# Kernel optimization log

Hardware: AMD Instinct MI355X
Metric: run time of the kernel (lower is better)

Reference implementation:

```python
import jax, jax.numpy as jnp
import numpy as np

N_EXPERTS, D_IN, D_OUT = 8, 1024, 1024
N_TOKENS = 8192


def setup_inputs() -> dict:
    key = jax.random.key(0)
    ks = jax.random.split(key, 5)
    s_in = 1.0 / np.sqrt(D_IN)
    x = jax.random.normal(ks[0], (N_TOKENS, D_IN), dtype=jnp.float32)
    W = jax.random.uniform(ks[1], (N_EXPERTS, D_IN, D_OUT), jnp.float32, -s_in, s_in)
    b = jax.random.uniform(ks[2], (N_EXPERTS, D_OUT), jnp.float32, -s_in, s_in)
    gate_W = jax.random.uniform(ks[3], (D_IN, N_EXPERTS), jnp.float32, -s_in, s_in)
    gate_b = jax.random.uniform(ks[4], (N_EXPERTS,), jnp.float32, -s_in, s_in)
    return {"x": x, "W": W, "b": b, "gate_W": gate_W, "gate_b": gate_b}


def reference(x, W, b, gate_W, gate_b):
    # gate: [n, e] softmax over experts
    gate_score = jax.nn.softmax(x @ gate_W + gate_b, axis=-1)
    # all experts applied densely: [n, e, o]
    expert_outputs = jnp.einsum('ni,eio->neo', x, W) + b[None, :, :]
    # weighted combine over expert axis: [n, o]
    return jnp.einsum('ne,neo->no', gate_score, expert_outputs)
```

## Files before the change

### kernel.cpp

```cpp
#include <hip/hip_runtime.h>
#include <hip/hip_bf16.h>
#include <cstdint>
#include <cstddef>

#define N_TOK 8192
#define D_IN  1024
#define D_OUT 1024
#define N_EXP 8
#define KTOT  (N_EXP * D_IN)

typedef __attribute__((ext_vector_type(8))) short short8;
typedef __attribute__((ext_vector_type(8))) unsigned short ushort8;
typedef __attribute__((ext_vector_type(4))) float f32x4;

__device__ __forceinline__ unsigned short f2bf(float f) {
    union { float f; unsigned int u; } v; v.f = f;
    return (unsigned short)((v.u + 0x7FFFu + ((v.u >> 16) & 1u)) >> 16);
}

__device__ __forceinline__ void load_lds16(const void* g, void* l) {
    __builtin_amdgcn_global_load_lds(
        (const __attribute__((address_space(1))) void*)g,
        (__attribute__((address_space(3))) void*)l,
        16, 0, 0);
}

__global__ __launch_bounds__(256) void prep_kernel(
    const float* __restrict__ x, const float* __restrict__ gW,
    const float* __restrict__ gbias, const float* __restrict__ W,
    unsigned short* __restrict__ xb, unsigned short* __restrict__ Wt,
    float* __restrict__ g_t) {
    const int b = blockIdx.x;
    const int t = threadIdx.x;

    if (b < 2048) {
        __shared__ float tile[64][65];
        const int e  = b >> 8;
        const int i0 = ((b >> 4) & 15) * 64;
        const int o0 = (b & 15) * 64;

        const int rr = t >> 4;
        const int rc = (t & 15) * 4;
#pragma unroll
        for (int j = 0; j < 4; ++j) {
            const float4 v = *(const float4*)(
                W + ((size_t)e * D_IN + (i0 + rr + 16 * j)) * D_OUT + o0 + rc);
            tile[rr + 16 * j][rc + 0] = v.x;
            tile[rr + 16 * j][rc + 1] = v.y;
            tile[rr + 16 * j][rc + 2] = v.z;
            tile[rr + 16 * j][rc + 3] = v.w;
        }
        __syncthreads();
        const int ow = t >> 2;
        const int c  = (t & 3) * 16;
        ushort8 v0, v1;
#pragma unroll
        for (int j = 0; j < 8; ++j) v0[j] = f2bf(tile[c + j][ow]);
#pragma unroll
        for (int j = 0; j < 8; ++j) v1[j] = f2bf(tile[c + 8 + j][ow]);
        unsigned short* dst = Wt + (size_t)(o0 + ow) * KTOT + e * D_IN + i0 + c;
        *(ushort8*)dst = v0;
        *(ushort8*)(dst + 8) = v1;
    } else {
        const int lane = t & 63;
        const int n    = (b - 2048) * 4 + (t >> 6);

        float acc[8];
#pragma unroll
        for (int e = 0; e < 8; ++e) acc[e] = 0.f;
#pragma unroll
        for (int jj = 0; jj < 4; ++jj) {
            const int i = 256 * jj + 4 * lane;
            const float4 xv = *(const float4*)(x + (size_t)n * D_IN + i);
            ushort4 u;
            u.x = f2bf(xv.x); u.y = f2bf(xv.y);
            u.z = f2bf(xv.z); u.w = f2bf(xv.w);
            *(ushort4*)(xb + (size_t)n * D_IN + i) = u;
            const float xs[4] = {xv.x, xv.y, xv.z, xv.w};
#pragma unroll
            for (int j = 0; j < 4; ++j) {
                const float* wr = gW + (size_t)(i + j) * N_EXP;
                const float4 w0 = *(const float4*)wr;
                const float4 w1 = *(const float4*)(wr + 4);
                acc[0] += xs[j] * w0.x; acc[1] += xs[j] * w0.y;
                acc[2] += xs[j] * w0.z; acc[3] += xs[j] * w0.w;
                acc[4] += xs[j] * w1.x; acc[5] += xs[j] * w1.y;
                acc[6] += xs[j] * w1.z; acc[7] += xs[j] * w1.w;
            }
        }
#pragma unroll
        for (int off = 32; off > 0; off >>= 1) {
#pragma unroll
            for (int e = 0; e < 8; ++e) acc[e] += __shfl_down(acc[e], off);
        }
        if (lane == 0) {
            float lg[8], mx = -1e30f;
#pragma unroll
            for (int e = 0; e < 8; ++e) {
                lg[e] = acc[e] + gbias[e];
                mx = fmaxf(mx, lg[e]);
            }
            float s = 0.f;
#pragma unroll
            for (int e = 0; e < 8; ++e) { lg[e] = expf(lg[e] - mx); s += lg[e]; }
            const float inv = 1.f / s;
#pragma unroll
            for (int e = 0; e < 8; ++e)
                g_t[(size_t)e * N_TOK + n] = lg[e] * inv;
        }
    }
}

__global__ __launch_bounds__(256, 2) void moe_gemm6_kernel(
    const unsigned short* __restrict__ xb,
    const unsigned short* __restrict__ Wt,
    const float* __restrict__ bias,
    const float* __restrict__ g_t,
    float* __restrict__ out) {
    __shared__ __align__(16) unsigned short Abuf[2][128 * 32];
    __shared__ __align__(16) unsigned short Bbuf[2][128 * 32];
    __shared__ __align__(16) float g_s[N_EXP][128];
    __shared__ __align__(16) float r_s[N_EXP][128];
    __shared__ __align__(16) float b_s[N_EXP][128];

    const int t    = threadIdx.x;
    const int lane = t & 63;
    const int ln15 = lane & 15;
    const int quad = lane >> 4;
    const int wave = t >> 6;
    const int wm0  = (wave >> 1) * 64;
    const int wn0  = (wave & 1) * 64;

    const int flat = blockIdx.x + 8 * blockIdx.y;
    const int xs_  = (flat >> 3) & 7;
    const int ys_  = ((flat & 7) << 3) | (flat >> 6);
    const int bn0  = xs_ * 128;
    const int bm0  = ys_ * 128;

    for (int j = t; j < N_EXP * 128; j += 256) {
        const int e = j >> 7, r = j & 127;
        g_s[e][r] = g_t[(size_t)e * N_TOK + bm0 + r];
        b_s[e][r] = bias[(size_t)e * D_OUT + bn0 + r];
    }
    __syncthreads();
    if (t < 128) {
        float d[N_EXP];
#pragma unroll
        for (int e = 0; e < N_EXP; ++e) d[e] = fmaxf(g_s[e][t], 1e-30f);
#pragma unroll
        for (int e = 1; e < N_EXP; ++e) r_s[e][t] = d[e - 1] / d[e];
        r_s[0][t] = d[N_EXP - 1];
    }

    f32x4 acc[4][4];
#pragma unroll
    for (int mi = 0; mi < 4; ++mi)
#pragma unroll
        for (int ni = 0; ni < 4; ++ni)
            acc[mi][ni] = (f32x4){0.f, 0.f, 0.f, 0.f};

    unsigned short* aL0[2] = {&Abuf[0][wave * 512], &Abuf[1][wave * 512]};
    unsigned short* aL1[2] = {&Abuf[0][2048 + wave * 512],
                              &Abuf[1][2048 + wave * 512]};
    unsigned short* bL0[2] = {&Bbuf[0][wave * 512], &Bbuf[1][wave * 512]};
    unsigned short* bL1[2] = {&Bbuf[0][2048 + wave * 512],
                              &Bbuf[1][2048 + wave * 512]};

    const int csw = ((t & 3) ^ ((t >> 3) & 3)) * 8;
    const unsigned short* ga =
        xb + (size_t)(bm0 + (t >> 2)) * D_IN + csw;
    const unsigned short* gbB =
        Wt + (size_t)(bn0 + (t >> 2)) * KTOT + csw;

    const int ksw = (quad ^ ((ln15 >> 1) & 3)) * 8;

    load_lds16(ga, aL0[0]);
    load_lds16(ga + 64 * D_IN, aL1[0]);
    load_lds16(gbB, bL0[0]);
    load_lds16(gbB + 64 * KTOT, bL1[0]);
    __syncthreads();

    for (int kt = 0; kt < 256; ++kt) {
        const int cb  = kt & 1;
        const int nb  = cb ^ 1;
        const int kt1 = (kt + 1) & 255;

        load_lds16(ga + (kt1 & 31) * 32,              aL0[nb]);
        load_lds16(ga + 64 * D_IN + (kt1 & 31) * 32,  aL1[nb]);
        load_lds16(gbB + kt1 * 32,                    bL0[nb]);
        load_lds16(gbB + 64 * KTOT + kt1 * 32,        bL1[nb]);

        if (kt && !(kt & 31)) {
            const int e = kt >> 5;
#pragma unroll
            for (int mi = 0; mi < 4; ++mi) {
                const f32x4 rv = *(const f32x4*)&r_s[e][wm0 + mi * 16 + quad * 4];
#pragma unroll
                for (int ni = 0; ni < 4; ++ni)
#pragma unroll
                    for (int r = 0; r < 4; ++r) acc[mi][ni][r] *= rv[r];
            }
        }

        short8 af[4], bv[4];
#pragma unroll
        for (int mi = 0; mi < 4; ++mi)
            af[mi] = *(const short8*)
                &Abuf[cb][(wm0 + mi * 16 + ln15) * 32 + ksw];
#pragma unroll
        for (int ni = 0; ni < 4; ++ni)
            bv[ni] = *(const short8*)
                &Bbuf[cb][(wn0 + ni * 16 + ln15) * 32 + ksw];
#pragma unroll
        for (int mi = 0; mi < 4; ++mi)
#pragma unroll
            for (int ni = 0; ni < 4; ++ni)
                acc[mi][ni] = __builtin_amdgcn_mfma_f32_16x16x32_bf16(
                    af[mi], bv[ni], acc[mi][ni], 0, 0, 0);

        __syncthreads();
    }

#pragma unroll
    for (int mi = 0; mi < 4; ++mi) {
        const f32x4 fin = *(const f32x4*)&r_s[0][wm0 + mi * 16 + quad * 4];
#pragma unroll
        for (int ni = 0; ni < 4; ++ni)
#pragma unroll
            for (int r = 0; r < 4; ++r) acc[mi][ni][r] *= fin[r];
    }
#pragma unroll
    for (int e = 0; e < N_EXP; ++e) {
        f32x4 gv[4];
        float bv[4];
#pragma unroll
        for (int mi = 0; mi < 4; ++mi)
            gv[mi] = *(const f32x4*)&g_s[e][wm0 + mi * 16 + quad * 4];
#pragma unroll
        for (int ni = 0; ni < 4; ++ni) bv[ni] = b_s[e][wn0 + ni * 16 + ln15];
#pragma unroll
        for (int mi = 0; mi < 4; ++mi)
#pragma unroll
            for (int ni = 0; ni < 4; ++ni)
#pragma unroll
                for (int r = 0; r < 4; ++r)
                    acc[mi][ni][r] += gv[mi][r] * bv[ni];
    }

#pragma unroll
    for (int mi = 0; mi < 4; ++mi) {
#pragma unroll
        for (int ni = 0; ni < 4; ++ni) {
            const int col  = bn0 + wn0 + ni * 16 + ln15;
            const int row0 = bm0 + wm0 + mi * 16 + quad * 4;
#pragma unroll
            for (int r = 0; r < 4; ++r)
                out[(size_t)(row0 + r) * D_OUT + col] = acc[mi][ni][r];
        }
    }
}

extern "C" void kernel_launch(void* const* d_in, const int* in_sizes, int n_in,
                              void* d_out, int out_size, void* d_ws, size_t ws_size,
                              hipStream_t stream) {
    const float* x  = (const float*)d_in[0];
    const float* W  = (const float*)d_in[1];
    const float* b  = (const float*)d_in[2];
    const float* gW = (const float*)d_in[3];
    const float* gb = (const float*)d_in[4];
    float* out = (float*)d_out;

    unsigned short* xb  = (unsigned short*)d_ws;
    unsigned short* Wt  = xb + (size_t)N_TOK * D_IN;
    float*          g_t = (float*)(Wt + (size_t)D_OUT * KTOT);

    prep_kernel<<<4096, 256, 0, stream>>>(x, gW, gb, W, xb, Wt, g_t);
    moe_gemm6_kernel<<<dim3(D_OUT / 128, N_TOK / 128), 256, 0, stream>>>(
        xb, Wt, b, g_t, out);
}
```

Before: 281.8 us.

## Pre-pack W into MFMA fragment panels and load B straight to registers

The prep kernel now writes the bf16 transposed weights as 16-column panels laid out in the MFMA B-operand fragment order. In the GEMM, each wave reads its B fragments directly from global memory into registers with a one-iteration register prefetch, and the B shared-memory double buffer is removed. The aim is to cut LDS traffic and LDS capacity pressure for the B operand. In exchange, the two waves that share a column half each read the same B data separately, and the global-load latency is hidden by only one iteration of prefetch. The final prefetch reads one panel step past the end of W.

```diff
diff --git a/kernel.cpp b/kernel.cpp
--- a/kernel.cpp
+++ b/kernel.cpp
@@ -8,6 +8,7 @@
 #define D_OUT 1024
 #define N_EXP 8
 #define KTOT  (N_EXP * D_IN)
+#define PANEL_ELEMS (KTOT * 16)
 
 typedef __attribute__((ext_vector_type(8))) short short8;
 typedef __attribute__((ext_vector_type(8))) unsigned short ushort8;
@@ -51,16 +52,19 @@
             tile[rr + 16 * j][rc + 3] = v.w;
         }
         __syncthreads();
-        const int ow = t >> 2;
-        const int c  = (t & 3) * 16;
+        const int ow  = t >> 2;
+        const int c   = (t & 3) * 16;
         ushort8 v0, v1;
 #pragma unroll
         for (int j = 0; j < 8; ++j) v0[j] = f2bf(tile[c + j][ow]);
 #pragma unroll
         for (int j = 0; j < 8; ++j) v1[j] = f2bf(tile[c + 8 + j][ow]);
-        unsigned short* dst = Wt + (size_t)(o0 + ow) * KTOT + e * D_IN + i0 + c;
+        const int col = o0 + ow;
+        const int kg  = e * D_IN + i0 + c;
+        unsigned short* dst = Wt + (size_t)(col >> 4) * PANEL_ELEMS
+                                 + (size_t)(kg >> 3) * 128 + (col & 15) * 8;
         *(ushort8*)dst = v0;
-        *(ushort8*)(dst + 8) = v1;
+        *(ushort8*)(dst + 128) = v1;
     } else {
         const int lane = t & 63;
         const int n    = (b - 2048) * 4 + (t >> 6);
@@ -111,14 +115,13 @@
     }
 }
 
-__global__ __launch_bounds__(256, 2) void moe_gemm6_kernel(
+__global__ __launch_bounds__(256, 2) void moe_gemm7_kernel(
     const unsigned short* __restrict__ xb,
     const unsigned short* __restrict__ Wt,
     const float* __restrict__ bias,
     const float* __restrict__ g_t,
     float* __restrict__ out) {
     __shared__ __align__(16) unsigned short Abuf[2][128 * 32];
-    __shared__ __align__(16) unsigned short Bbuf[2][128 * 32];
     __shared__ __align__(16) float g_s[N_EXP][128];
     __shared__ __align__(16) float r_s[N_EXP][128];
     __shared__ __align__(16) float b_s[N_EXP][128];
@@ -162,33 +165,33 @@
     unsigned short* aL0[2] = {&Abuf[0][wave * 512], &Abuf[1][wave * 512]};
     unsigned short* aL1[2] = {&Abuf[0][2048 + wave * 512],
                               &Abuf[1][2048 + wave * 512]};
-    unsigned short* bL0[2] = {&Bbuf[0][wave * 512], &Bbuf[1][wave * 512]};
-    unsigned short* bL1[2] = {&Bbuf[0][2048 + wave * 512],
-                              &Bbuf[1][2048 + wave * 512]};
-
     const int csw = ((t & 3) ^ ((t >> 3) & 3)) * 8;
     const unsigned short* ga =
         xb + (size_t)(bm0 + (t >> 2)) * D_IN + csw;
-    const unsigned short* gbB =
-        Wt + (size_t)(bn0 + (t >> 2)) * KTOT + csw;
-
     const int ksw = (quad ^ ((ln15 >> 1) & 3)) * 8;
+
+    const unsigned short* gB[4];
+#pragma unroll
+    for (int ni = 0; ni < 4; ++ni)
+        gB[ni] = Wt + (size_t)(((bn0 + wn0) >> 4) + ni) * PANEL_ELEMS + lane * 8;
 
     load_lds16(ga, aL0[0]);
     load_lds16(ga + 64 * D_IN, aL1[0]);
-    load_lds16(gbB, bL0[0]);
-    load_lds16(gbB + 64 * KTOT, bL1[0]);
+    short8 bcur[4], bnxt[4];
+#pragma unroll
+    for (int ni = 0; ni < 4; ++ni) bcur[ni] = *(const short8*)gB[ni];
     __syncthreads();
 
     for (int kt = 0; kt < 256; ++kt) {
         const int cb  = kt & 1;
         const int nb  = cb ^ 1;
-        const int kt1 = (kt + 1) & 255;
-
-        load_lds16(ga + (kt1 & 31) * 32,              aL0[nb]);
-        load_lds16(ga + 64 * D_IN + (kt1 & 31) * 32,  aL1[nb]);
-        load_lds16(gbB + kt1 * 32,                    bL0[nb]);
-        load_lds16(gbB + 64 * KTOT + kt1 * 32,        bL1[nb]);
+        const int kt1 = kt + 1;
+
+        load_lds16(ga + ((kt1 & 255) & 31) * 32,             aL0[nb]);
+        load_lds16(ga + 64 * D_IN + ((kt1 & 255) & 31) * 32, aL1[nb]);
+#pragma unroll
+        for (int ni = 0; ni < 4; ++ni)
+            bnxt[ni] = *(const short8*)(gB[ni] + (size_t)kt1 * 512);
 
         if (kt && !(kt & 31)) {
             const int e = kt >> 5;
@@ -202,23 +205,21 @@
             }
         }
 
-        short8 af[4], bv[4];
+        short8 af[4];
 #pragma unroll
         for (int mi = 0; mi < 4; ++mi)
             af[mi] = *(const short8*)
                 &Abuf[cb][(wm0 + mi * 16 + ln15) * 32 + ksw];
 #pragma unroll
-        for (int ni = 0; ni < 4; ++ni)
-            bv[ni] = *(const short8*)
-                &Bbuf[cb][(wn0 + ni * 16 + ln15) * 32 + ksw];
-#pragma unroll
         for (int mi = 0; mi < 4; ++mi)
 #pragma unroll
             for (int ni = 0; ni < 4; ++ni)
                 acc[mi][ni] = __builtin_amdgcn_mfma_f32_16x16x32_bf16(
-                    af[mi], bv[ni], acc[mi][ni], 0, 0, 0);
+                    af[mi], bcur[ni], acc[mi][ni], 0, 0, 0);
 
         __syncthreads();
+#pragma unroll
+        for (int ni = 0; ni < 4; ++ni) bcur[ni] = bnxt[ni];
     }
 
 #pragma unroll
@@ -275,6 +276,6 @@
     float*          g_t = (float*)(Wt + (size_t)D_OUT * KTOT);
 
     prep_kernel<<<4096, 256, 0, stream>>>(x, gW, gb, W, xb, Wt, g_t);
-    moe_gemm6_kernel<<<dim3(D_OUT / 128, N_TOK / 128), 256, 0, stream>>>(
+    moe_gemm7_kernel<<<dim3(D_OUT / 128, N_TOK / 128), 256, 0, stream>>>(
         xb, Wt, b, g_t, out);
 }
```

New measurement: 307.5 us. +9.1%, slower.
